# Performance work log

Hardware: AMD Instinct MI355X
Metric: run time of the kernel (lower is better)

Reference implementation:

```python
import jax, jax.numpy as jnp
import numpy as np

N = 100000   # nodes
E = 1600000  # edges (avg degree 16)
IN = 128     # in_channels
H = 64       # num_hidden -> conv1 out = 2*H = 128
RRELU_SLOPE = (1.0 / 8.0 + 1.0 / 3.0) / 2.0  # F.rrelu eval: mean of (lower, upper)


def setup_inputs() -> dict:
    key = jax.random.key(0)
    k1, k2, k3, k4 = jax.random.split(key, 4)
    x = jax.random.normal(k1, (N, IN), dtype=jnp.float32)
    edge_index = jax.random.randint(k2, (2, E), 0, N, dtype=jnp.int32)
    # Glorot-ish init for the two GCN linear layers (PyG GCNConv has weight + bias)
    W1 = jax.random.normal(k3, (IN, 2 * H), dtype=jnp.float32) * (1.0 / np.sqrt(IN))
    b1 = jnp.zeros((2 * H,), dtype=jnp.float32)
    W2 = jax.random.normal(k4, (2 * H, H), dtype=jnp.float32) * (1.0 / np.sqrt(2 * H))
    b2 = jnp.zeros((H,), dtype=jnp.float32)
    return {"x": x, "edge_index": edge_index, "W1": W1, "b1": b1, "W2": W2, "b2": b2}


def _gcn_conv(x, row, col, norm, W, b, n):
    # PyG GCNConv: transform, gather source nodes, scale by sym norm, scatter-add to targets
    h = x @ W                                   # [N, out]
    msg = h[row] * norm[:, None]                # [E+N, out] gathered messages
    return jax.ops.segment_sum(msg, col, num_segments=n) + b


def reference(x, edge_index, W1, b1, W2, b2):
    n = x.shape[0]
    loops = jnp.arange(n, dtype=edge_index.dtype)
    row = jnp.concatenate([edge_index[0], loops])  # sources (with self-loops)
    col = jnp.concatenate([edge_index[1], loops])  # targets (with self-loops)
    deg = jax.ops.segment_sum(jnp.ones_like(col, dtype=x.dtype), col, num_segments=n)
    dinv = jnp.where(deg > 0, jax.lax.rsqrt(deg), 0.0)
    norm = dinv[row] * dinv[col]                  # deg^{-1/2}[u] * deg^{-1/2}[v]
    h = _gcn_conv(x, row, col, norm, W1, b1, n)
    h = jnp.where(h >= 0, h, RRELU_SLOPE * h)     # rrelu (eval mode)
    return _gcn_conv(h, row, col, norm, W2, b2, n)
```

## Files before the change

### kernel.cpp

```cpp
#include <hip/hip_runtime.h>


#define C_IN   128
#define C_MID  128
#define C_OUT2 64
#define SLOT_CAP 64
#define NWIN   8

typedef __attribute__((ext_vector_type(8))) short short8;
typedef __attribute__((ext_vector_type(4))) float floatx4;

__device__ __constant__ float kSlope = 0.22916666666666666f;

__device__ __forceinline__ unsigned short f2bf(float f) {
    unsigned u = __builtin_bit_cast(unsigned, f);
    u = (u + 0x7fffu + ((u >> 16) & 1u)) >> 16;
    return (unsigned short)u;
}
__device__ __forceinline__ float bf2f(unsigned short h) {
    return __builtin_bit_cast(float, (unsigned)h << 16);
}

__global__ void fill_kernel(const int* __restrict__ ei, int* __restrict__ cnt,
                            int* __restrict__ slots, int E, int chunk) {
    int win = blockIdx.x & (NWIN - 1);
    int blk = blockIdx.x >> 3;
    int e = blk * 256 + threadIdx.x;
    if (e >= E) return;
    int v = ei[E + e];
    if ((unsigned)(v - win * chunk) >= (unsigned)chunk) return;
    int u = ei[e];
    int pos = atomicAdd(&cnt[v], 1);
    if (pos < SLOT_CAP) slots[(size_t)v * SLOT_CAP + pos] = u;
}

__global__ void dinv_kernel(const int* __restrict__ cnt, float* __restrict__ dinv, int n) {
    int v = blockIdx.x * 256 + threadIdx.x;
    if (v >= n) return;
    dinv[v] = rsqrtf((float)(cnt[v] + 1));
}

__global__ void prep_w(const float* __restrict__ W1, const float* __restrict__ W2,
                       ushort* __restrict__ W1T, ushort* __restrict__ W2T) {
    int t = blockIdx.x * 256 + threadIdx.x;
    if (t < C_MID * C_IN) {
        int nn = t >> 7, k = t & 127;
        W1T[t] = f2bf(W1[k * C_MID + nn]);
    } else {
        int i = t - C_MID * C_IN;
        if (i < C_OUT2 * C_MID) {
            int nn = i >> 7, k = i & 127;
            W2T[i] = f2bf(W2[k * C_OUT2 + nn]);
        }
    }
}

template <int CO, bool ABF>
__global__ __launch_bounds__(256) void gemm_mfma(const void* __restrict__ Xv,
                                                 const ushort* __restrict__ WT,
                                                 ushort* __restrict__ Y, int n) {
    constexpr int LDW = 136;
    constexpr int NT = CO / 16;
    __shared__ __align__(16) ushort Ws[CO * LDW];
    const int tid = threadIdx.x, wave = tid >> 6, lane = tid & 63;
    const int m = lane & 15, q = lane >> 4;
    const int row0 = blockIdx.x * 64;

#pragma unroll
    for (int c = 0; c < CO / 16; ++c) {
        int id = tid + c * 256;
        int r = id >> 4, h8 = id & 15;
        *(int4*)&Ws[r * LDW + h8 * 8] = ((const int4*)(WT + r * C_IN))[h8];
    }
    __syncthreads();

    const int rowA = min(row0 + wave * 16 + m, n - 1);
    floatx4 acc[NT];
#pragma unroll
    for (int c = 0; c < NT; ++c) acc[c] = (floatx4){0.f, 0.f, 0.f, 0.f};

#pragma unroll
    for (int s = 0; s < 4; ++s) {
        short8 af;
        if constexpr (ABF) {
            af = *(const short8*)((const ushort*)Xv + (size_t)rowA * C_IN + s * 32 + q * 8);
        } else {
            const float* xp = (const float*)Xv + (size_t)rowA * C_IN + s * 32 + q * 8;
            float4 a0 = *(const float4*)xp;
            float4 a1 = *(const float4*)(xp + 4);
            union { unsigned short us[8]; short8 v; } t;
            t.us[0] = f2bf(a0.x); t.us[1] = f2bf(a0.y); t.us[2] = f2bf(a0.z); t.us[3] = f2bf(a0.w);
            t.us[4] = f2bf(a1.x); t.us[5] = f2bf(a1.y); t.us[6] = f2bf(a1.z); t.us[7] = f2bf(a1.w);
            af = t.v;
        }
#pragma unroll
        for (int c = 0; c < NT; ++c) {
            short8 bf = *(short8*)&Ws[(c * 16 + m) * LDW + s * 32 + q * 8];
            acc[c] = __builtin_amdgcn_mfma_f32_16x16x32_bf16(af, bf, acc[c], 0, 0, 0);
        }
    }
#pragma unroll
    for (int c = 0; c < NT; ++c)
#pragma unroll
        for (int i = 0; i < 4; ++i) {
            int rr = row0 + wave * 16 + q * 4 + i;
            if (rr < n) Y[(size_t)rr * CO + c * 16 + m] = f2bf(acc[c][i]);
        }
}

template <int C, bool DO_RRELU, bool OUT_BF>
__global__ __launch_bounds__(256) void agg_kernel(const ushort* __restrict__ H,
                                                  const int* __restrict__ slots,
                                                  const int* __restrict__ cnt,
                                                  const float* __restrict__ dinv,
                                                  const float* __restrict__ bias,
                                                  void* __restrict__ outv, int n) {
    constexpr int CPL = C / 64;
    const int wave = threadIdx.x >> 6, lane = threadIdx.x & 63;
    const int v = blockIdx.x * 4 + wave;
    if (v >= n) return;

    const float dv = dinv[v];
    int deg = cnt[v];
    if (deg > SLOT_CAP) deg = SLOT_CAP;

    const int* sl = slots + (size_t)v * SLOT_CAP;
    int u_l = (lane < deg) ? sl[lane] : 0;
    float w_l = dinv[u_l] * dv;

    float acc[CPL];
    {
        unsigned short hv[CPL];
        __builtin_memcpy(hv, H + (size_t)v * C + lane * CPL, CPL * 2);
#pragma unroll
        for (int p = 0; p < CPL; ++p) acc[p] = bf2f(hv[p]) * (dv * dv);
    }

    int j = 0;
    for (; j + 4 <= deg; j += 4) {
        int u0 = __shfl(u_l, j + 0), u1 = __shfl(u_l, j + 1);
        int u2 = __shfl(u_l, j + 2), u3 = __shfl(u_l, j + 3);
        float w0 = __shfl(w_l, j + 0), w1 = __shfl(w_l, j + 1);
        float w2 = __shfl(w_l, j + 2), w3 = __shfl(w_l, j + 3);
        unsigned short a0[CPL], a1[CPL], a2[CPL], a3[CPL];
        __builtin_memcpy(a0, H + (size_t)u0 * C + lane * CPL, CPL * 2);
        __builtin_memcpy(a1, H + (size_t)u1 * C + lane * CPL, CPL * 2);
        __builtin_memcpy(a2, H + (size_t)u2 * C + lane * CPL, CPL * 2);
        __builtin_memcpy(a3, H + (size_t)u3 * C + lane * CPL, CPL * 2);
#pragma unroll
        for (int p = 0; p < CPL; ++p)
            acc[p] += bf2f(a0[p]) * w0 + bf2f(a1[p]) * w1 + bf2f(a2[p]) * w2 + bf2f(a3[p]) * w3;
    }
    for (; j < deg; ++j) {
        int u = __shfl(u_l, j);
        float w = __shfl(w_l, j);
        unsigned short a[CPL];
        __builtin_memcpy(a, H + (size_t)u * C + lane * CPL, CPL * 2);
#pragma unroll
        for (int p = 0; p < CPL; ++p) acc[p] += bf2f(a[p]) * w;
    }

#pragma unroll
    for (int p = 0; p < CPL; ++p) {
        float r = acc[p] + bias[lane * CPL + p];
        if (DO_RRELU) r = (r >= 0.f) ? r : r * kSlope;
        if constexpr (OUT_BF) ((ushort*)outv)[(size_t)v * C + lane * CPL + p] = f2bf(r);
        else                  ((float*)outv)[(size_t)v * C + lane * CPL + p] = r;
    }
}

extern "C" void kernel_launch(void* const* d_in, const int* in_sizes, int n_in,
                              void* d_out, int out_size, void* d_ws, size_t ws_size,
                              hipStream_t stream) {
    const float* x  = (const float*)d_in[0];
    const int*   ei = (const int*)d_in[1];
    const float* W1 = (const float*)d_in[2];
    const float* b1 = (const float*)d_in[3];
    const float* W2 = (const float*)d_in[4];
    const float* b2 = (const float*)d_in[5];
    const int n = in_sizes[0] / C_IN;
    const int E = in_sizes[1] / 2;

    char* w = (char*)d_ws;
    auto alloc = [&](size_t bytes) -> char* {
        char* p = w; w += (bytes + 255) & ~(size_t)255; return p;
    };
    int*    cnt   = (int*)alloc((size_t)n * 4);
    float*  dinv  = (float*)alloc((size_t)n * 4);
    int*    slots = (int*)alloc((size_t)n * SLOT_CAP * 4);
    ushort* h1    = (ushort*)alloc((size_t)n * C_MID * 2);
    ushort* h2    = (ushort*)alloc((size_t)n * C_MID * 2);
    ushort* h3    = h1;
    ushort* W1T   = (ushort*)alloc((size_t)C_MID * C_IN * 2);
    ushort* W2T   = (ushort*)alloc((size_t)C_OUT2 * C_MID * 2);

    const int bpp = (E + 255) / 256;
    const int chunk = (n + NWIN - 1) / NWIN;

    hipMemsetAsync(cnt, 0, (size_t)n * 4, stream);
    prep_w<<<96, 256, 0, stream>>>(W1, W2, W1T, W2T);
    fill_kernel<<<bpp * NWIN, 256, 0, stream>>>(ei, cnt, slots, E, chunk);
    dinv_kernel<<<(n + 255) / 256, 256, 0, stream>>>(cnt, dinv, n);
    gemm_mfma<C_MID, false><<<(n + 63) / 64, 256, 0, stream>>>(x, W1T, h1, n);
    agg_kernel<C_MID, true, true><<<(n + 3) / 4, 256, 0, stream>>>(h1, slots, cnt, dinv, b1, h2, n);
    gemm_mfma<C_OUT2, true><<<(n + 63) / 64, 256, 0, stream>>>(h2, W2T, h3, n);
    agg_kernel<C_OUT2, false, false><<<(n + 3) / 4, 256, 0, stream>>>(h3, slots, cnt, dinv, b2, d_out, n);
}
```

Baseline: 317.4 us.

## Split aggregation wave into neighbor groups with 16-byte gathers; batch edge loads in fill

The aggregation kernel now splits each wave into groups of lanes. Each group gathers a whole neighbor row using 16-byte vector loads, so several neighbors are processed in parallel, and the partial sums are combined with a cross-lane xor-shuffle reduction. The self-loop is folded in as an extra slot. The fill kernel has each thread handle 8 edges, loading them first with nontemporal loads and then doing the atomics, which cuts the block count. This trades more reduction shuffles and lower output-store parallelism (only one group writes) for wider and fewer memory transactions.

```diff
diff --git a/kernel.cpp b/kernel.cpp
--- a/kernel.cpp
+++ b/kernel.cpp
@@ -6,6 +6,7 @@
 #define C_OUT2 64
 #define SLOT_CAP 64
 #define NWIN   8
+#define EPB    2048
 
 typedef __attribute__((ext_vector_type(8))) short short8;
 typedef __attribute__((ext_vector_type(4))) float floatx4;
@@ -17,21 +18,34 @@
     u = (u + 0x7fffu + ((u >> 16) & 1u)) >> 16;
     return (unsigned short)u;
 }
-__device__ __forceinline__ float bf2f(unsigned short h) {
-    return __builtin_bit_cast(float, (unsigned)h << 16);
+__device__ __forceinline__ float bflo(int x) {
+    return __builtin_bit_cast(float, (unsigned)x << 16);
+}
+__device__ __forceinline__ float bfhi(int x) {
+    return __builtin_bit_cast(float, (unsigned)(x & 0xffff0000));
 }
 
 __global__ void fill_kernel(const int* __restrict__ ei, int* __restrict__ cnt,
                             int* __restrict__ slots, int E, int chunk) {
-    int win = blockIdx.x & (NWIN - 1);
-    int blk = blockIdx.x >> 3;
-    int e = blk * 256 + threadIdx.x;
-    if (e >= E) return;
-    int v = ei[E + e];
-    if ((unsigned)(v - win * chunk) >= (unsigned)chunk) return;
-    int u = ei[e];
-    int pos = atomicAdd(&cnt[v], 1);
-    if (pos < SLOT_CAP) slots[(size_t)v * SLOT_CAP + pos] = u;
+    const int win = blockIdx.x & (NWIN - 1);
+    const int blk = blockIdx.x >> 3;
+    const int base = blk * EPB + threadIdx.x;
+    int vs[8], us[8];
+#pragma unroll
+    for (int k = 0; k < 8; ++k) {
+        int e = base + k * 256;
+        bool ok = e < E;
+        vs[k] = ok ? __builtin_nontemporal_load(ei + E + e) : -1;
+        us[k] = ok ? __builtin_nontemporal_load(ei + e) : 0;
+    }
+#pragma unroll
+    for (int k = 0; k < 8; ++k) {
+        int v = vs[k];
+        if ((unsigned)(v - win * chunk) < (unsigned)chunk) {
+            int pos = atomicAdd(&cnt[v], 1);
+            if (pos < SLOT_CAP) slots[(size_t)v * SLOT_CAP + pos] = us[k];
+        }
+    }
 }
 
 __global__ void dinv_kernel(const int* __restrict__ cnt, float* __restrict__ dinv, int n) {
@@ -115,7 +129,8 @@
                                                   const float* __restrict__ dinv,
                                                   const float* __restrict__ bias,
                                                   void* __restrict__ outv, int n) {
-    constexpr int CPL = C / 64;
+    constexpr int GS = C / 8;
+    constexpr int NG = 64 / GS;
     const int wave = threadIdx.x >> 6, lane = threadIdx.x & 63;
     const int v = blockIdx.x * 4 + wave;
     if (v >= n) return;
@@ -125,47 +140,53 @@
     if (deg > SLOT_CAP) deg = SLOT_CAP;
 
     const int* sl = slots + (size_t)v * SLOT_CAP;
-    int u_l = (lane < deg) ? sl[lane] : 0;
-    float w_l = dinv[u_l] * dv;
-
-    float acc[CPL];
-    {
-        unsigned short hv[CPL];
-        __builtin_memcpy(hv, H + (size_t)v * C + lane * CPL, CPL * 2);
-#pragma unroll
-        for (int p = 0; p < CPL; ++p) acc[p] = bf2f(hv[p]) * (dv * dv);
-    }
-
-    int j = 0;
-    for (; j + 4 <= deg; j += 4) {
-        int u0 = __shfl(u_l, j + 0), u1 = __shfl(u_l, j + 1);
-        int u2 = __shfl(u_l, j + 2), u3 = __shfl(u_l, j + 3);
-        float w0 = __shfl(w_l, j + 0), w1 = __shfl(w_l, j + 1);
-        float w2 = __shfl(w_l, j + 2), w3 = __shfl(w_l, j + 3);
-        unsigned short a0[CPL], a1[CPL], a2[CPL], a3[CPL];
-        __builtin_memcpy(a0, H + (size_t)u0 * C + lane * CPL, CPL * 2);
-        __builtin_memcpy(a1, H + (size_t)u1 * C + lane * CPL, CPL * 2);
-        __builtin_memcpy(a2, H + (size_t)u2 * C + lane * CPL, CPL * 2);
-        __builtin_memcpy(a3, H + (size_t)u3 * C + lane * CPL, CPL * 2);
-#pragma unroll
-        for (int p = 0; p < CPL; ++p)
-            acc[p] += bf2f(a0[p]) * w0 + bf2f(a1[p]) * w1 + bf2f(a2[p]) * w2 + bf2f(a3[p]) * w3;
-    }
-    for (; j < deg; ++j) {
-        int u = __shfl(u_l, j);
-        float w = __shfl(w_l, j);
-        unsigned short a[CPL];
-        __builtin_memcpy(a, H + (size_t)u * C + lane * CPL, CPL * 2);
-#pragma unroll
-        for (int p = 0; p < CPL; ++p) acc[p] += bf2f(a[p]) * w;
-    }
-
-#pragma unroll
-    for (int p = 0; p < CPL; ++p) {
-        float r = acc[p] + bias[lane * CPL + p];
-        if (DO_RRELU) r = (r >= 0.f) ? r : r * kSlope;
-        if constexpr (OUT_BF) ((ushort*)outv)[(size_t)v * C + lane * CPL + p] = f2bf(r);
-        else                  ((float*)outv)[(size_t)v * C + lane * CPL + p] = r;
+    int u_l = (lane < deg) ? sl[lane] : v;
+    float w_l = (lane < deg) ? dinv[u_l] * dv : (lane == deg ? dv * dv : 0.f);
+
+    int lim = deg + 1;
+    if (lim > 64) lim = 64;
+
+    const int g = lane / GS, s = lane % GS;
+    float acc[8];
+#pragma unroll
+    for (int k = 0; k < 8; ++k) acc[k] = 0.f;
+
+    for (int j = 0; j < lim; j += NG) {
+        int jj = j + g;
+        int jc = jj < 63 ? jj : 63;
+        int u = __shfl(u_l, jc);
+        float ws = __shfl(w_l, jc);
+        float w = (jj < lim) ? ws : 0.f;
+        const int4 d = *(const int4*)(H + (size_t)u * C + s * 8);
+        acc[0] += bflo(d.x) * w; acc[1] += bfhi(d.x) * w;
+        acc[2] += bflo(d.y) * w; acc[3] += bfhi(d.y) * w;
+        acc[4] += bflo(d.z) * w; acc[5] += bfhi(d.z) * w;
+        acc[6] += bflo(d.w) * w; acc[7] += bfhi(d.w) * w;
+    }
+
+#pragma unroll
+    for (int k = 0; k < 8; ++k)
+#pragma unroll
+        for (int off = GS; off < 64; off <<= 1)
+            acc[k] += __shfl_xor(acc[k], off);
+
+    if (g == 0) {
+        float r[8];
+#pragma unroll
+        for (int k = 0; k < 8; ++k) {
+            r[k] = acc[k] + bias[s * 8 + k];
+            if (DO_RRELU) r[k] = (r[k] >= 0.f) ? r[k] : r[k] * kSlope;
+        }
+        if constexpr (OUT_BF) {
+            union { ushort us[8]; int4 v; } o;
+#pragma unroll
+            for (int k = 0; k < 8; ++k) o.us[k] = f2bf(r[k]);
+            *(int4*)((ushort*)outv + (size_t)v * C + s * 8) = o.v;
+        } else {
+            float* op = (float*)outv + (size_t)v * C + s * 8;
+            *(float4*)op       = (float4){r[0], r[1], r[2], r[3]};
+            *(float4*)(op + 4) = (float4){r[4], r[5], r[6], r[7]};
+        }
     }
 }
 
@@ -194,12 +215,12 @@
     ushort* W1T   = (ushort*)alloc((size_t)C_MID * C_IN * 2);
     ushort* W2T   = (ushort*)alloc((size_t)C_OUT2 * C_MID * 2);
 
-    const int bpp = (E + 255) / 256;
     const int chunk = (n + NWIN - 1) / NWIN;
+    const int fill_blocks = ((E + EPB - 1) / EPB) * NWIN;
 
     hipMemsetAsync(cnt, 0, (size_t)n * 4, stream);
     prep_w<<<96, 256, 0, stream>>>(W1, W2, W1T, W2T);
-    fill_kernel<<<bpp * NWIN, 256, 0, stream>>>(ei, cnt, slots, E, chunk);
+    fill_kernel<<<fill_blocks, 256, 0, stream>>>(ei, cnt, slots, E, chunk);
     dinv_kernel<<<(n + 255) / 256, 256, 0, stream>>>(cnt, dinv, n);
     gemm_mfma<C_MID, false><<<(n + 63) / 64, 256, 0, stream>>>(x, W1T, h1, n);
     agg_kernel<C_MID, true, true><<<(n + 3) / 4, 256, 0, stream>>>(h1, slots, cnt, dinv, b1, h2, n);
```

New measurement: 314.6 us. Within noise of the previous version (-0.9%).
